# Kernel tuning notes

Hardware: AMD Instinct MI355X
Metric: run time of the kernel (lower is better)

The kernel has to match this reference:

```python
import jax, jax.numpy as jnp
import numpy as np

B, N, DIM = 4, 1024, 1024
HEADS, DH = 16, 64
INNER = HEADS * DH          # 1024
PROJ_H = max(16, DH // 8)   # 16
TOP_K = 256
TEMP = 1.0
SCALE = DH ** -0.5
LN_EPS = 1e-5


def setup_inputs() -> dict:
    key = jax.random.key(0)
    ks = jax.random.split(key, 9)
    s = 0.02
    return {
        "x": jax.random.normal(ks[0], (B, N, DIM), dtype=jnp.float32),
        "w_qkv": jax.random.normal(ks[1], (3 * INNER, DIM), dtype=jnp.float32) * s,
        "w_out": jax.random.normal(ks[2], (DIM, INNER), dtype=jnp.float32) * s,
        "b_out": jnp.zeros((DIM,), dtype=jnp.float32),
        "ln_g": jnp.ones((DH,), dtype=jnp.float32),
        "ln_b": jnp.zeros((DH,), dtype=jnp.float32),
        "w1": jax.random.normal(ks[3], (PROJ_H, DH), dtype=jnp.float32) * s,
        "b1": jnp.zeros((PROJ_H,), dtype=jnp.float32),
        "w2": jax.random.normal(ks[4], (1, PROJ_H), dtype=jnp.float32) * s,
        "b2": jnp.zeros((1,), dtype=jnp.float32),
    }


def _soma_gate(token_feat, ln_g, ln_b, w1, b1, w2, b2):
    # token_feat: [B, N, DH] -> gate [B, N] in (0,1)
    mu = token_feat.mean(axis=-1, keepdims=True)
    var = token_feat.var(axis=-1, keepdims=True)
    H = (token_feat - mu) * jax.lax.rsqrt(var + LN_EPS) * ln_g + ln_b
    h = jax.nn.gelu(H @ w1.T + b1, approximate=False)
    scores = (h @ w2.T + b2)[..., 0]                       # [B, N]
    scores = scores / (TEMP + 1e-12)
    # top-k soft mask: non-topk positions set to -1e9 before sigmoid
    topk_vals, topk_idx = jax.lax.top_k(scores, TOP_K)
    b_idx = jnp.arange(scores.shape[0])[:, None]
    scores = jnp.full_like(scores, -1e9).at[b_idx, topk_idx].set(topk_vals)
    return jax.nn.sigmoid(scores)


def reference(x, w_qkv, w_out, b_out, ln_g, ln_b, w1, b1, w2, b2):
    Bx, Nx, _ = x.shape
    qkv = x @ w_qkv.T                                      # [B, N, 3*INNER]
    q, k, v = jnp.split(qkv, 3, axis=-1)
    to_heads = lambda t: t.reshape(Bx, Nx, HEADS, DH).transpose(0, 2, 1, 3)
    q, k, v = to_heads(q), to_heads(k), to_heads(v)        # [B, H, N, DH]

    dots = jnp.einsum('bhid,bhjd->bhij', q, k) * SCALE     # [B, H, N, N]

    q_mean = q.mean(axis=1)                                # [B, N, DH]
    gate = _soma_gate(q_mean, ln_g, ln_b, w1, b1, w2, b2)  # [B, N]
    dots = dots * (gate[:, None, :, None] * gate[:, None, None, :])

    attn = jax.nn.softmax(dots, axis=-1)
    out = jnp.einsum('bhij,bhjd->bhid', attn, v)           # [B, H, N, DH]
    out = out.transpose(0, 2, 1, 3).reshape(Bx, Nx, INNER)
    return out @ w_out.T + b_out
```

## Files before the change

kernel.cpp:

```cpp
#include <hip/hip_runtime.h>
#include <hip/hip_bf16.h>
#include <stdint.h>

typedef __bf16 bf16;
typedef __bf16 bf16x8 __attribute__((ext_vector_type(8)));
typedef float floatx4 __attribute__((ext_vector_type(4)));

typedef const __attribute__((address_space(1))) uint32_t glb_u32;
typedef __attribute__((address_space(3))) uint32_t lds_u32;

__device__ __forceinline__ void cp16(void* lds, const void* gp) {
    __builtin_amdgcn_global_load_lds((glb_u32*)gp, (lds_u32*)lds, 16, 0, 0);
}

#define MFMA16(a, b, c) __builtin_amdgcn_mfma_f32_16x16x32_bf16((a), (b), (c), 0, 0, 0)
#define SCALE_ 0.125f

__global__ __launch_bounds__(256) void k_cvt_prep(
    const float* __restrict__ x, const float* __restrict__ wq,
    const float* __restrict__ wo, bf16* __restrict__ xb,
    bf16* __restrict__ wqb, bf16* __restrict__ wob,
    float* __restrict__ wqmT) {
    if (blockIdx.x < 4096) {
        size_t i8 = ((size_t)blockIdx.x * 256 + threadIdx.x) * 8;
        const float* src; bf16* dst; size_t off;
        if (i8 < 4194304)      { src = x;  dst = xb;  off = i8; }
        else if (i8 < 7340032) { src = wq; dst = wqb; off = i8 - 4194304; }
        else                   { src = wo; dst = wob; off = i8 - 7340032; }
        float4 a = *(const float4*)(src + off);
        float4 b = *(const float4*)(src + off + 4);
        union { bf16 h[8]; uint4 u; } tmp;
        tmp.h[0] = (bf16)a.x; tmp.h[1] = (bf16)a.y; tmp.h[2] = (bf16)a.z; tmp.h[3] = (bf16)a.w;
        tmp.h[4] = (bf16)b.x; tmp.h[5] = (bf16)b.y; tmp.h[6] = (bf16)b.z; tmp.h[7] = (bf16)b.w;
        *(uint4*)(dst + off) = tmp.u;
    } else {
        int t = (blockIdx.x - 4096) * 256 + threadIdx.x;
        int k = t & 1023, d = t >> 10;
        float s = 0.f;
        #pragma unroll
        for (int h = 0; h < 16; ++h) s += wq[(size_t)(h * 64 + d) * 1024 + k];
        wqmT[k * 64 + d] = s * (1.f / 16.f);
    }
}

__global__ __launch_bounds__(256) void k_score(
    const float* __restrict__ xf, const float* __restrict__ wqmT,
    const float* __restrict__ lng, const float* __restrict__ lnb,
    const float* __restrict__ w1f, const float* __restrict__ b1f,
    const float* __restrict__ w2f, const float* __restrict__ b2f,
    float* __restrict__ scores) {
    const int w = threadIdx.x >> 6, lane = threadIdx.x & 63;
    const int r0 = blockIdx.x * 8;
    const int k0 = w * 256;
    __shared__ float part[4][8][64];
    __shared__ float qm_s[8][64];
    __shared__ float Hs[4][64];
    __shared__ float hh[4][16];

    float acc[8];
    #pragma unroll
    for (int i = 0; i < 8; ++i) acc[i] = 0.f;

    for (int k = k0; k < k0 + 256; k += 4) {
        float w0 = wqmT[(k + 0) * 64 + lane];
        float w1 = wqmT[(k + 1) * 64 + lane];
        float w2 = wqmT[(k + 2) * 64 + lane];
        float w3 = wqmT[(k + 3) * 64 + lane];
        #pragma unroll
        for (int i = 0; i < 8; ++i) {
            float4 xv = *(const float4*)(xf + (size_t)(r0 + i) * 1024 + k);
            acc[i] += xv.x * w0; acc[i] += xv.y * w1;
            acc[i] += xv.z * w2; acc[i] += xv.w * w3;
        }
    }
    #pragma unroll
    for (int i = 0; i < 8; ++i) part[w][i][lane] = acc[i];
    __syncthreads();
    for (int e = threadIdx.x; e < 512; e += 256) {
        int r = e >> 6, d = e & 63;
        qm_s[r][d] = part[0][r][d] + part[1][r][d] + part[2][r][d] + part[3][r][d];
    }
    __syncthreads();

    for (int i = 0; i < 2; ++i) {
        const int r = w * 2 + i;
        float qm = qm_s[r][lane];
        float s = qm;
        #pragma unroll
        for (int off = 32; off > 0; off >>= 1) s += __shfl_xor(s, off);
        float mu = s * (1.f / 64.f);
        float dx = qm - mu;
        float v2 = dx * dx;
        #pragma unroll
        for (int off = 32; off > 0; off >>= 1) v2 += __shfl_xor(v2, off);
        float var = v2 * (1.f / 64.f);
        float H = dx * (1.0f / sqrtf(var + 1e-5f)) * lng[lane] + lnb[lane];
        Hs[w][lane] = H;
        if (lane < 16) {
            float a = b1f[lane];
            #pragma unroll
            for (int d = 0; d < 64; ++d) a += Hs[w][d] * w1f[lane * 64 + d];
            hh[w][lane] = 0.5f * a * (1.0f + erff(a * 0.70710678118654752f));
        }
        if (lane == 0) {
            float sc = b2f[0];
            #pragma unroll
            for (int p = 0; p < 16; ++p) sc += hh[w][p] * w2f[p];
            scores[r0 + r] = sc;
        }
    }
}

__global__ __launch_bounds__(256) void k_topk(const float* __restrict__ scores,
                                              float* __restrict__ gate,
                                              int* __restrict__ idx,
                                              float* __restrict__ gsel) {
    const int w = threadIdx.x >> 6, lane = threadIdx.x & 63;
    const float* sc = scores + w * 1024;
    float s[16];
    uint32_t key[16];
    #pragma unroll
    for (int i = 0; i < 16; ++i) {
        s[i] = sc[lane * 16 + i];
        uint32_t u = __float_as_uint(s[i]);
        key[i] = (u >> 31) ? ~u : (u | 0x80000000u);
    }
    uint32_t prefix = 0;
    for (int bit = 31; bit >= 0; --bit) {
        uint32_t cand = prefix | (1u << bit);
        int c = 0;
        #pragma unroll
        for (int i = 0; i < 16; ++i) c += (key[i] >= cand);
        #pragma unroll
        for (int off = 1; off < 64; off <<= 1) c += __shfl_xor(c, off);
        if (c >= 256) prefix = cand;
    }
    int cg = 0, eq = 0;
    #pragma unroll
    for (int i = 0; i < 16; ++i) { cg += (key[i] > prefix); eq += (key[i] == prefix); }
    #pragma unroll
    for (int off = 1; off < 64; off <<= 1) cg += __shfl_xor(cg, off);
    const int quota = 256 - cg;
    int xs = eq;
    #pragma unroll
    for (int off = 1; off < 64; off <<= 1) {
        int y = __shfl_up(xs, off);
        if (lane >= off) xs += y;
    }
    int run = xs - eq;
    bool selv[16];
    int cnt = 0;
    #pragma unroll
    for (int i = 0; i < 16; ++i) {
        bool sel = key[i] > prefix;
        if (key[i] == prefix) { sel = (run < quota); run++; }
        selv[i] = sel;
        cnt += sel ? 1 : 0;
        gate[w * 1024 + lane * 16 + i] = sel ? 1.0f / (1.0f + expf(-s[i])) : 0.0f;
    }
    int xc = cnt;
    #pragma unroll
    for (int off = 1; off < 64; off <<= 1) {
        int y = __shfl_up(xc, off);
        if (lane >= off) xc += y;
    }
    int pos = xc - cnt;
    #pragma unroll
    for (int i = 0; i < 16; ++i) {
        if (selv[i]) {
            idx[w * 256 + pos]  = lane * 16 + i;
            gsel[w * 256 + pos] = 1.0f / (1.0f + expf(-s[i]));
            pos++;
        }
    }
}

__global__ __launch_bounds__(256) void k_qkv_fast(
    const bf16* __restrict__ xb, const bf16* __restrict__ wqb,
    bf16* __restrict__ qbuf, bf16* __restrict__ kbuf, bf16* __restrict__ vbuf) {
    __shared__ bf16 As[128 * 32];
    __shared__ bf16 Bs[128 * 32];
    const int t = threadIdx.x;
    const int lane = t & 63;
    const int w = t >> 6;
    const int n0 = blockIdx.x * 128;
    const int m0 = blockIdx.y * 128;
    const bf16* Asrc = xb + (size_t)m0 * 1024;
    const bf16* Bsrc = wqb + (size_t)n0 * 1024;

    const int srow = t >> 2;
    const int scol = (t & 3) * 8;
    const int wm = (w & 1) * 64;
    const int wn = (w >> 1) * 64;
    const int fr = lane & 15;
    const int kc = (lane >> 4) * 8;

    floatx4 zero4 = {0.f, 0.f, 0.f, 0.f};
    floatx4 acc[4][4];
    #pragma unroll
    for (int i = 0; i < 4; ++i)
        #pragma unroll
        for (int j = 0; j < 4; ++j) acc[i][j] = zero4;

    for (int k0 = 0; k0 < 1024; k0 += 32) {
        __syncthreads();
        cp16(As + t * 8,        Asrc + (size_t)srow * 1024 + k0 + scol);
        cp16(As + t * 8 + 2048, Asrc + (size_t)(srow + 64) * 1024 + k0 + scol);
        cp16(Bs + t * 8,        Bsrc + (size_t)srow * 1024 + k0 + scol);
        cp16(Bs + t * 8 + 2048, Bsrc + (size_t)(srow + 64) * 1024 + k0 + scol);
        __syncthreads();
        bf16x8 a[4], b[4];
        #pragma unroll
        for (int mi = 0; mi < 4; ++mi)
            a[mi] = *(const bf16x8*)&As[(wm + mi * 16 + fr) * 32 + kc];
        #pragma unroll
        for (int ni = 0; ni < 4; ++ni)
            b[ni] = *(const bf16x8*)&Bs[(wn + ni * 16 + fr) * 32 + kc];
        #pragma unroll
        for (int mi = 0; mi < 4; ++mi)
            #pragma unroll
            for (int ni = 0; ni < 4; ++ni)
                acc[mi][ni] = MFMA16(a[mi], b[ni], acc[mi][ni]);
    }

    const int rowb = (lane >> 4) * 4;
    #pragma unroll
    for (int ni = 0; ni < 4; ++ni) {
        const int n_base = n0 + wn + ni * 16;
        const int region = n_base >> 10;
        const int nn = n_base & 1023;
        const int h = nn >> 6;
        const int d = (nn & 63) + fr;
        bf16* dst = (region == 0) ? qbuf : (region == 1) ? kbuf : vbuf;
        #pragma unroll
        for (int mi = 0; mi < 4; ++mi) {
            #pragma unroll
            for (int r = 0; r < 4; ++r) {
                const int mg = m0 + wm + mi * 16 + rowb + r;
                const int bb = mg >> 10;
                const int nq = mg & 1023;
                const size_t bh = (size_t)(bb * 16 + h);
                dst[(bh * 1024 + nq) * 64 + d] = (bf16)acc[mi][ni][r];
            }
        }
    }
}

__global__ __launch_bounds__(256) void k_compact(
    const bf16* __restrict__ kbuf, const bf16* __restrict__ vbuf,
    const int* __restrict__ idx, bf16* __restrict__ Ksel,
    bf16* __restrict__ VselT, float* __restrict__ SumVuns) {
    const int bh = blockIdx.x, b = bh >> 4;
    const int t = threadIdx.x, w = t >> 6, lane = t & 63;
    const bf16* kb = kbuf + (size_t)bh * 65536;
    const bf16* vb = vbuf + (size_t)bh * 65536;
    bf16* Ko = Ksel + (size_t)bh * 16384;
    bf16* Vo = VselT + (size_t)bh * 16384;

    __shared__ bf16 Vt[64][72];
    __shared__ float redAll[4][64];
    __shared__ float redSel[4][64];

    float sAll = 0.f;
    for (int j = w * 256; j < w * 256 + 256; ++j)
        sAll += (float)vb[(size_t)j * 64 + lane];
    redAll[w][lane] = sAll;

    const int d = t & 63, sg = t >> 6;
    const int s_loc = t >> 2, part = t & 3;
    float sSel = 0.f;

    for (int c = 0; c < 4; ++c) {
        __syncthreads();
        int j = idx[b * 256 + c * 64 + s_loc];
        const uint4* ksrc = (const uint4*)(kb + (size_t)j * 64 + part * 16);
        uint4* kdst = (uint4*)(Ko + (size_t)(c * 64 + s_loc) * 64 + part * 16);
        kdst[0] = ksrc[0]; kdst[1] = ksrc[1];
        const uint4* vsrc = (const uint4*)(vb + (size_t)j * 64 + part * 16);
        uint4 v0 = vsrc[0], v1 = vsrc[1];
        *(uint4*)&Vt[s_loc][part * 16]     = v0;
        *(uint4*)&Vt[s_loc][part * 16 + 8] = v1;
        __syncthreads();
        union { bf16 h[16]; uint4 u[2]; } tmp;
        #pragma unroll
        for (int u = 0; u < 16; ++u) {
            bf16 v = Vt[sg * 16 + u][d];
            tmp.h[u] = v;
            sSel += (float)v;
        }
        uint4* vdst = (uint4*)(Vo + (size_t)d * 256 + c * 64 + sg * 16);
        vdst[0] = tmp.u[0]; vdst[1] = tmp.u[1];
    }
    redSel[sg][d] = sSel;
    __syncthreads();
    if (t < 64) {
        float su = redAll[0][t] + redAll[1][t] + redAll[2][t] + redAll[3][t]
                 - (redSel[0][t] + redSel[1][t] + redSel[2][t] + redSel[3][t]);
        SumVuns[bh * 64 + t] = su;
    }
}

__global__ __launch_bounds__(256) void k_attn(
    bf16* __restrict__ qbuf, const bf16* __restrict__ Ksel,
    const bf16* __restrict__ VselT, const float* __restrict__ gate,
    const float* __restrict__ gsel, const float* __restrict__ SumVuns) {
    const int bh = blockIdx.x;
    const int qt = blockIdx.y;
    const int b = bh >> 4;
    const int t = threadIdx.x, w = t >> 6, lane = t & 63;
    const int m0 = qt * 64;
    bf16* qb = qbuf + (size_t)bh * 65536;
    const bf16* kb = Ksel + (size_t)bh * 16384;
    const bf16* vb = VselT + (size_t)bh * 16384;

    __shared__ bf16 Qs[64 * 72];
    __shared__ bf16 Ks[64 * 72];
    __shared__ bf16 Vs[64 * 72];
    __shared__ bf16 Ps[4][16 * 72];

    #pragma unroll
    for (int c = 0; c < 2; ++c) {
        int idx2 = t + 256 * c, row = idx2 >> 3, c8 = (idx2 & 7) * 8;
        *(uint4*)&Qs[row * 72 + c8] = *(const uint4*)&qb[(size_t)(m0 + row) * 64 + c8];
    }
    const int fr = lane & 15;
    const int kq = lane >> 4;
    const int rowb = kq * 4;
    __syncthreads();
    bf16x8 aq[2];
    aq[0] = *(const bf16x8*)&Qs[(w * 16 + fr) * 72 + kq * 8];
    aq[1] = *(const bf16x8*)&Qs[(w * 16 + fr) * 72 + 32 + kq * 8];

    float gq[4];
    #pragma unroll
    for (int r = 0; r < 4; ++r)
        gq[r] = gate[b * 1024 + m0 + w * 16 + rowb + r] * SCALE_;

    float mrow[4] = {0.f, 0.f, 0.f, 0.f};
    float lrow[4] = {0.f, 0.f, 0.f, 0.f};
    floatx4 zero4 = {0.f, 0.f, 0.f, 0.f};
    floatx4 Of[4] = {zero4, zero4, zero4, zero4};

    for (int jt = 0; jt < 4; ++jt) {
        const int j0 = jt * 64;
        __syncthreads();
        #pragma unroll
        for (int c = 0; c < 2; ++c) {
            int idx2 = t + 256 * c, row = idx2 >> 3, c8 = (idx2 & 7) * 8;
            *(uint4*)&Ks[row * 72 + c8] = *(const uint4*)&kb[(size_t)(j0 + row) * 64 + c8];
            *(uint4*)&Vs[row * 72 + c8] = *(const uint4*)&vb[(size_t)row * 256 + j0 + c8];
        }
        __syncthreads();

        floatx4 S[4] = {zero4, zero4, zero4, zero4};
        #pragma unroll
        for (int ks = 0; ks < 2; ++ks) {
            #pragma unroll
            for (int ni = 0; ni < 4; ++ni) {
                bf16x8 bfr = *(const bf16x8*)&Ks[(ni * 16 + fr) * 72 + ks * 32 + kq * 8];
                S[ni] = MFMA16(aq[ks], bfr, S[ni]);
            }
        }
        float gk[4];
        #pragma unroll
        for (int ni = 0; ni < 4; ++ni) gk[ni] = gsel[b * 256 + j0 + ni * 16 + fr];

        float p[4][4], rmax[4] = {0.f, 0.f, 0.f, 0.f};
        #pragma unroll
        for (int ni = 0; ni < 4; ++ni)
            #pragma unroll
            for (int r = 0; r < 4; ++r) {
                float sv = S[ni][r] * (gq[r] * gk[ni]);
                p[ni][r] = sv;
                rmax[r] = fmaxf(rmax[r], sv);
            }
        #pragma unroll
        for (int r = 0; r < 4; ++r) {
            #pragma unroll
            for (int off = 1; off < 16; off <<= 1)
                rmax[r] = fmaxf(rmax[r], __shfl_xor(rmax[r], off));
        }
        float alpha[4], rsum[4] = {0.f, 0.f, 0.f, 0.f};
        #pragma unroll
        for (int r = 0; r < 4; ++r) {
            float mn = fmaxf(mrow[r], rmax[r]);
            alpha[r] = __expf(mrow[r] - mn);
            mrow[r] = mn;
        }
        #pragma unroll
        for (int ni = 0; ni < 4; ++ni)
            #pragma unroll
            for (int r = 0; r < 4; ++r) {
                float pv = __expf(p[ni][r] - mrow[r]);
                p[ni][r] = pv;
                rsum[r] += pv;
            }
        #pragma unroll
        for (int r = 0; r < 4; ++r) {
            #pragma unroll
            for (int off = 1; off < 16; off <<= 1) rsum[r] += __shfl_xor(rsum[r], off);
            lrow[r] = lrow[r] * alpha[r] + rsum[r];
        }
        #pragma unroll
        for (int nd = 0; nd < 4; ++nd)
            #pragma unroll
            for (int r = 0; r < 4; ++r) Of[nd][r] *= alpha[r];

        #pragma unroll
        for (int ni = 0; ni < 4; ++ni)
            #pragma unroll
            for (int r = 0; r < 4; ++r)
                Ps[w][(rowb + r) * 72 + ni * 16 + fr] = (bf16)p[ni][r];

        #pragma unroll
        for (int ks = 0; ks < 2; ++ks) {
            bf16x8 ap = *(const bf16x8*)&Ps[w][fr * 72 + ks * 32 + kq * 8];
            #pragma unroll
            for (int nd = 0; nd < 4; ++nd) {
                bf16x8 bv = *(const bf16x8*)&Vs[(nd * 16 + fr) * 72 + ks * 32 + kq * 8];
                Of[nd] = MFMA16(ap, bv, Of[nd]);
            }
        }
    }

    #pragma unroll
    for (int nd = 0; nd < 4; ++nd)
        #pragma unroll
        for (int r = 0; r < 4; ++r) {
            float em = __expf(-mrow[r]);
            float num = Of[nd][r] + em * SumVuns[bh * 64 + nd * 16 + fr];
            float den = lrow[r] + 768.0f * em;
            qb[(size_t)(m0 + w * 16 + rowb + r) * 64 + nd * 16 + fr] = (bf16)(num / den);
        }
}

__global__ __launch_bounds__(256) void k_out_fast(
    const bf16* __restrict__ A, const bf16* __restrict__ wob,
    const float* __restrict__ b_out, float* __restrict__ out) {
    __shared__ bf16 As[128 * 32];
    __shared__ bf16 Bs[128 * 32];
    const int t = threadIdx.x;
    const int lane = t & 63;
    const int w = t >> 6;
    const int n0 = blockIdx.x * 128;
    const int m0 = blockIdx.y * 128;
    const bf16* Bsrc = wob + (size_t)n0 * 1024;

    const int srow = t >> 2;
    const int scol = (t & 3) * 8;
    const int wm = (w & 1) * 64;
    const int wn = (w >> 1) * 64;
    const int fr = lane & 15;
    const int kc = (lane >> 4) * 8;

    const int mg1 = m0 + srow, mg2 = m0 + srow + 64;
    const size_t abase1 = ((size_t)(mg1 >> 10) * 16 * 1024 + (mg1 & 1023)) * 64;
    const size_t abase2 = ((size_t)(mg2 >> 10) * 16 * 1024 + (mg2 & 1023)) * 64;

    floatx4 zero4 = {0.f, 0.f, 0.f, 0.f};
    floatx4 acc[4][4];
    #pragma unroll
    for (int i = 0; i < 4; ++i)
        #pragma unroll
        for (int j = 0; j < 4; ++j) acc[i][j] = zero4;

    for (int k0 = 0; k0 < 1024; k0 += 32) {
        __syncthreads();
        {
            const int kk = k0 + scol;
            const size_t hoff = (size_t)(kk >> 6) * 65536 + (kk & 63);
            cp16(As + t * 8,        A + abase1 + hoff);
            cp16(As + t * 8 + 2048, A + abase2 + hoff);
        }
        cp16(Bs + t * 8,        Bsrc + (size_t)srow * 1024 + k0 + scol);
        cp16(Bs + t * 8 + 2048, Bsrc + (size_t)(srow + 64) * 1024 + k0 + scol);
        __syncthreads();
        bf16x8 a[4], b[4];
        #pragma unroll
        for (int mi = 0; mi < 4; ++mi)
            a[mi] = *(const bf16x8*)&As[(wm + mi * 16 + fr) * 32 + kc];
        #pragma unroll
        for (int ni = 0; ni < 4; ++ni)
            b[ni] = *(const bf16x8*)&Bs[(wn + ni * 16 + fr) * 32 + kc];
        #pragma unroll
        for (int mi = 0; mi < 4; ++mi)
            #pragma unroll
            for (int ni = 0; ni < 4; ++ni)
                acc[mi][ni] = MFMA16(a[mi], b[ni], acc[mi][ni]);
    }

    const int rowb = (lane >> 4) * 4;
    #pragma unroll
    for (int ni = 0; ni < 4; ++ni) {
        const int ng = n0 + wn + ni * 16 + fr;
        const float bias = b_out[ng];
        #pragma unroll
        for (int mi = 0; mi < 4; ++mi)
            #pragma unroll
            for (int r = 0; r < 4; ++r) {
                const int mg = m0 + wm + mi * 16 + rowb + r;
                out[(size_t)mg * 1024 + ng] = acc[mi][ni][r] + bias;
            }
    }
}

extern "C" void kernel_launch(void* const* d_in, const int* in_sizes, int n_in,
                              void* d_out, int out_size, void* d_ws, size_t ws_size,
                              hipStream_t stream) {
    const float* x     = (const float*)d_in[0];
    const float* w_qkv = (const float*)d_in[1];
    const float* w_out = (const float*)d_in[2];
    const float* b_out = (const float*)d_in[3];
    const float* ln_g  = (const float*)d_in[4];
    const float* ln_b  = (const float*)d_in[5];
    const float* w1    = (const float*)d_in[6];
    const float* b1    = (const float*)d_in[7];
    const float* w2    = (const float*)d_in[8];
    const float* b2    = (const float*)d_in[9];
    float* out = (float*)d_out;

    char* ws = (char*)d_ws;
    bf16*  qbuf  = (bf16*)(ws);
    bf16*  kbuf  = (bf16*)(ws + 8388608);
    bf16*  vbuf  = (bf16*)(ws + 16777216);
    bf16*  xb    = (bf16*)(ws + 25165824);
    bf16*  wqb   = (bf16*)(ws + 33554432);
    bf16*  wob   = (bf16*)(ws + 39845888);
    bf16*  Ksel    = (bf16*)(ws + 33554432);
    bf16*  VselT   = (bf16*)(ws + 35651584);
    float* SumVuns = (float*)(ws + 37748736);
    const size_t tail = 41943040;
    float* wqmT   = (float*)(ws + tail);
    int*   idx    = (int*)(ws + tail);
    float* gsel   = (float*)(ws + tail + 4096);
    float* scores = (float*)(ws + tail + 262144);
    float* gate   = (float*)(ws + tail + 262144 + 16384);

    k_cvt_prep<<<4352, 256, 0, stream>>>(x, w_qkv, w_out, xb, wqb, wob, wqmT);
    k_score<<<512, 256, 0, stream>>>(x, wqmT, ln_g, ln_b, w1, b1, w2, b2, scores);
    k_topk<<<1, 256, 0, stream>>>(scores, gate, idx, gsel);
    k_qkv_fast<<<dim3(24, 32), 256, 0, stream>>>(xb, wqb, qbuf, kbuf, vbuf);
    k_compact<<<64, 256, 0, stream>>>(kbuf, vbuf, idx, Ksel, VselT, SumVuns);
    k_attn<<<dim3(64, 16), 256, 0, stream>>>(qbuf, Ksel, VselT, gate, gsel, SumVuns);
    k_out_fast<<<dim3(8, 32), 256, 0, stream>>>(qbuf, wob, b_out, out);
}
```

Measured before the change: 241.9 us.

## Compute Q/K projections, attention and output projection only for top-k tokens

```diff
diff --git a/kernel.cpp b/kernel.cpp
--- a/kernel.cpp
+++ b/kernel.cpp
@@ -175,19 +175,15 @@
     }
 }
 
-__global__ __launch_bounds__(256) void k_qkv_fast(
+__global__ __launch_bounds__(256) void k_qkv_sel(
     const bf16* __restrict__ xb, const bf16* __restrict__ wqb,
-    bf16* __restrict__ qbuf, bf16* __restrict__ kbuf, bf16* __restrict__ vbuf) {
+    const int* __restrict__ idx, bf16* __restrict__ qsel,
+    bf16* __restrict__ ksel, bf16* __restrict__ vbuf) {
     __shared__ bf16 As[128 * 32];
     __shared__ bf16 Bs[128 * 32];
     const int t = threadIdx.x;
     const int lane = t & 63;
     const int w = t >> 6;
-    const int n0 = blockIdx.x * 128;
-    const int m0 = blockIdx.y * 128;
-    const bf16* Asrc = xb + (size_t)m0 * 1024;
-    const bf16* Bsrc = wqb + (size_t)n0 * 1024;
-
     const int srow = t >> 2;
     const int scol = (t & 3) * 8;
     const int wm = (w & 1) * 64;
@@ -195,6 +191,29 @@
     const int fr = lane & 15;
     const int kc = (lane >> 4) * 8;
 
+    const int bid = blockIdx.x;
+    const bool isV = bid < 256;
+    int n0, m0;
+    size_t abase1, abase2;
+    const bf16* Bsrc;
+    if (isV) {
+        n0 = (bid & 7) * 128;
+        m0 = (bid >> 3) * 128;
+        Bsrc = wqb + (size_t)(2048 + n0) * 1024;
+        abase1 = (size_t)(m0 + srow) * 1024;
+        abase2 = (size_t)(m0 + srow + 64) * 1024;
+    } else {
+        int q = bid - 256;
+        n0 = (q & 15) * 128;
+        m0 = (q >> 4) * 128;
+        Bsrc = wqb + (size_t)n0 * 1024;
+        const int mg1 = m0 + srow, mg2 = mg1 + 64;
+        const int tok1 = idx[(mg1 >> 8) * 256 + (mg1 & 255)];
+        const int tok2 = idx[(mg2 >> 8) * 256 + (mg2 & 255)];
+        abase1 = ((size_t)(mg1 >> 8) * 1024 + tok1) * 1024;
+        abase2 = ((size_t)(mg2 >> 8) * 1024 + tok2) * 1024;
+    }
+
     floatx4 zero4 = {0.f, 0.f, 0.f, 0.f};
     floatx4 acc[4][4];
     #pragma unroll
@@ -204,8 +223,8 @@
 
     for (int k0 = 0; k0 < 1024; k0 += 32) {
         __syncthreads();
-        cp16(As + t * 8,        Asrc + (size_t)srow * 1024 + k0 + scol);
-        cp16(As + t * 8 + 2048, Asrc + (size_t)(srow + 64) * 1024 + k0 + scol);
+        cp16(As + t * 8,        xb + abase1 + k0 + scol);
+        cp16(As + t * 8 + 2048, xb + abase2 + k0 + scol);
         cp16(Bs + t * 8,        Bsrc + (size_t)srow * 1024 + k0 + scol);
         cp16(Bs + t * 8 + 2048, Bsrc + (size_t)(srow + 64) * 1024 + k0 + scol);
         __syncthreads();
@@ -227,34 +246,47 @@
     #pragma unroll
     for (int ni = 0; ni < 4; ++ni) {
         const int n_base = n0 + wn + ni * 16;
-        const int region = n_base >> 10;
-        const int nn = n_base & 1023;
-        const int h = nn >> 6;
-        const int d = (nn & 63) + fr;
-        bf16* dst = (region == 0) ? qbuf : (region == 1) ? kbuf : vbuf;
-        #pragma unroll
-        for (int mi = 0; mi < 4; ++mi) {
-            #pragma unroll
-            for (int r = 0; r < 4; ++r) {
-                const int mg = m0 + wm + mi * 16 + rowb + r;
-                const int bb = mg >> 10;
-                const int nq = mg & 1023;
-                const size_t bh = (size_t)(bb * 16 + h);
-                dst[(bh * 1024 + nq) * 64 + d] = (bf16)acc[mi][ni][r];
-            }
-        }
-    }
-}
-
-__global__ __launch_bounds__(256) void k_compact(
-    const bf16* __restrict__ kbuf, const bf16* __restrict__ vbuf,
-    const int* __restrict__ idx, bf16* __restrict__ Ksel,
-    bf16* __restrict__ VselT, float* __restrict__ SumVuns) {
-    const int bh = blockIdx.x, b = bh >> 4;
+        if (isV) {
+            const int h = n_base >> 6;
+            const int dd = (n_base & 63) + fr;
+            #pragma unroll
+            for (int mi = 0; mi < 4; ++mi)
+                #pragma unroll
+                for (int r = 0; r < 4; ++r) {
+                    const int mg = m0 + wm + mi * 16 + rowb + r;
+                    const int bb = mg >> 10, nq = mg & 1023;
+                    vbuf[(((size_t)(bb * 16 + h)) * 1024 + nq) * 64 + dd] =
+                        (bf16)acc[mi][ni][r];
+                }
+        } else {
+            const int region = n_base >> 10;
+            const int nn = n_base & 1023;
+            const int h = nn >> 6;
+            const int dd = (nn & 63) + fr;
+            #pragma unroll
+            for (int mi = 0; mi < 4; ++mi)
+                #pragma unroll
+                for (int r = 0; r < 4; ++r) {
+                    const int mg = m0 + wm + mi * 16 + rowb + r;
+                    const bf16 v = (bf16)acc[mi][ni][r];
+                    if (region == 0) {
+                        qsel[(size_t)mg * 1024 + h * 64 + dd] = v;
+                    } else {
+                        const int b = mg >> 8, s = mg & 255;
+                        ksel[(((size_t)(b * 16 + h)) * 256 + s) * 64 + dd] = v;
+                    }
+                }
+        }
+    }
+}
+
+__global__ __launch_bounds__(256) void k_vgather(
+    const bf16* __restrict__ vbuf, const int* __restrict__ idx,
+    bf16* __restrict__ VselT, float* __restrict__ SumVuns,
+    bf16* __restrict__ qsel) {
+    const int bh = blockIdx.x, b = bh >> 4, h = bh & 15;
     const int t = threadIdx.x, w = t >> 6, lane = t & 63;
-    const bf16* kb = kbuf + (size_t)bh * 65536;
     const bf16* vb = vbuf + (size_t)bh * 65536;
-    bf16* Ko = Ksel + (size_t)bh * 16384;
     bf16* Vo = VselT + (size_t)bh * 16384;
 
     __shared__ bf16 Vt[64][72];
@@ -273,19 +305,16 @@
     for (int c = 0; c < 4; ++c) {
         __syncthreads();
         int j = idx[b * 256 + c * 64 + s_loc];
-        const uint4* ksrc = (const uint4*)(kb + (size_t)j * 64 + part * 16);
-        uint4* kdst = (uint4*)(Ko + (size_t)(c * 64 + s_loc) * 64 + part * 16);
-        kdst[0] = ksrc[0]; kdst[1] = ksrc[1];
         const uint4* vsrc = (const uint4*)(vb + (size_t)j * 64 + part * 16);
         uint4 v0 = vsrc[0], v1 = vsrc[1];
         *(uint4*)&Vt[s_loc][part * 16]     = v0;
         *(uint4*)&Vt[s_loc][part * 16 + 8] = v1;
         __syncthreads();
-        union { bf16 h[16]; uint4 u[2]; } tmp;
+        union { bf16 h_[16]; uint4 u[2]; } tmp;
         #pragma unroll
         for (int u = 0; u < 16; ++u) {
             bf16 v = Vt[sg * 16 + u][d];
-            tmp.h[u] = v;
+            tmp.h_[u] = v;
             sSel += (float)v;
         }
         uint4* vdst = (uint4*)(Vo + (size_t)d * 256 + c * 64 + sg * 16);
@@ -294,22 +323,22 @@
     redSel[sg][d] = sSel;
     __syncthreads();
     if (t < 64) {
-        float su = redAll[0][t] + redAll[1][t] + redAll[2][t] + redAll[3][t]
-                 - (redSel[0][t] + redSel[1][t] + redSel[2][t] + redSel[3][t]);
-        SumVuns[bh * 64 + t] = su;
+        float sa = redAll[0][t] + redAll[1][t] + redAll[2][t] + redAll[3][t];
+        float ss = redSel[0][t] + redSel[1][t] + redSel[2][t] + redSel[3][t];
+        SumVuns[bh * 64 + t] = sa - ss;
+        qsel[(size_t)(1024 + b) * 1024 + h * 64 + t] = (bf16)(sa * (1.f / 1024.f));
     }
 }
 
 __global__ __launch_bounds__(256) void k_attn(
-    bf16* __restrict__ qbuf, const bf16* __restrict__ Ksel,
-    const bf16* __restrict__ VselT, const float* __restrict__ gate,
-    const float* __restrict__ gsel, const float* __restrict__ SumVuns) {
+    bf16* __restrict__ qsel, const bf16* __restrict__ Ksel,
+    const bf16* __restrict__ VselT, const float* __restrict__ gsel,
+    const float* __restrict__ SumVuns) {
     const int bh = blockIdx.x;
     const int qt = blockIdx.y;
-    const int b = bh >> 4;
+    const int b = bh >> 4, h = bh & 15;
     const int t = threadIdx.x, w = t >> 6, lane = t & 63;
     const int m0 = qt * 64;
-    bf16* qb = qbuf + (size_t)bh * 65536;
     const bf16* kb = Ksel + (size_t)bh * 16384;
     const bf16* vb = VselT + (size_t)bh * 16384;
 
@@ -321,7 +350,8 @@
     #pragma unroll
     for (int c = 0; c < 2; ++c) {
         int idx2 = t + 256 * c, row = idx2 >> 3, c8 = (idx2 & 7) * 8;
-        *(uint4*)&Qs[row * 72 + c8] = *(const uint4*)&qb[(size_t)(m0 + row) * 64 + c8];
+        *(uint4*)&Qs[row * 72 + c8] =
+            *(const uint4*)&qsel[(size_t)(b * 256 + m0 + row) * 1024 + h * 64 + c8];
     }
     const int fr = lane & 15;
     const int kq = lane >> 4;
@@ -334,7 +364,7 @@
     float gq[4];
     #pragma unroll
     for (int r = 0; r < 4; ++r)
-        gq[r] = gate[b * 1024 + m0 + w * 16 + rowb + r] * SCALE_;
+        gq[r] = gsel[b * 256 + m0 + w * 16 + rowb + r] * SCALE_;
 
     float mrow[4] = {0.f, 0.f, 0.f, 0.f};
     float lrow[4] = {0.f, 0.f, 0.f, 0.f};
@@ -430,13 +460,15 @@
             float em = __expf(-mrow[r]);
             float num = Of[nd][r] + em * SumVuns[bh * 64 + nd * 16 + fr];
             float den = lrow[r] + 768.0f * em;
-            qb[(size_t)(m0 + w * 16 + rowb + r) * 64 + nd * 16 + fr] = (bf16)(num / den);
-        }
-}
-
-__global__ __launch_bounds__(256) void k_out_fast(
+            qsel[(size_t)(b * 256 + m0 + w * 16 + rowb + r) * 1024 +
+                 h * 64 + nd * 16 + fr] = (bf16)(num / den);
+        }
+}
+
+__global__ __launch_bounds__(256) void k_out_sel(
     const bf16* __restrict__ A, const bf16* __restrict__ wob,
-    const float* __restrict__ b_out, float* __restrict__ out) {
+    const float* __restrict__ b_out, const int* __restrict__ idx,
+    float* __restrict__ ubase, float* __restrict__ out) {
     __shared__ bf16 As[128 * 32];
     __shared__ bf16 Bs[128 * 32];
     const int t = threadIdx.x;
@@ -453,10 +485,6 @@
     const int fr = lane & 15;
     const int kc = (lane >> 4) * 8;
 
-    const int mg1 = m0 + srow, mg2 = m0 + srow + 64;
-    const size_t abase1 = ((size_t)(mg1 >> 10) * 16 * 1024 + (mg1 & 1023)) * 64;
-    const size_t abase2 = ((size_t)(mg2 >> 10) * 16 * 1024 + (mg2 & 1023)) * 64;
-
     floatx4 zero4 = {0.f, 0.f, 0.f, 0.f};
     floatx4 acc[4][4];
     #pragma unroll
@@ -466,12 +494,8 @@
 
     for (int k0 = 0; k0 < 1024; k0 += 32) {
         __syncthreads();
-        {
-            const int kk = k0 + scol;
-            const size_t hoff = (size_t)(kk >> 6) * 65536 + (kk & 63);
-            cp16(As + t * 8,        A + abase1 + hoff);
-            cp16(As + t * 8 + 2048, A + abase2 + hoff);
-        }
+        cp16(As + t * 8,        A + (size_t)(m0 + srow) * 1024 + k0 + scol);
+        cp16(As + t * 8 + 2048, A + (size_t)(m0 + srow + 64) * 1024 + k0 + scol);
         cp16(Bs + t * 8,        Bsrc + (size_t)srow * 1024 + k0 + scol);
         cp16(Bs + t * 8 + 2048, Bsrc + (size_t)(srow + 64) * 1024 + k0 + scol);
         __syncthreads();
@@ -499,9 +523,26 @@
             #pragma unroll
             for (int r = 0; r < 4; ++r) {
                 const int mg = m0 + wm + mi * 16 + rowb + r;
-                out[(size_t)mg * 1024 + ng] = acc[mi][ni][r] + bias;
+                const float val = acc[mi][ni][r] + bias;
+                if (mg < 1024) {
+                    const int b = mg >> 8, s = mg & 255;
+                    const int tok = idx[b * 256 + s];
+                    out[((size_t)b * 1024 + tok) * 1024 + ng] = val;
+                } else if (mg < 1028) {
+                    ubase[(size_t)(mg - 1024) * 1024 + ng] = val;
+                }
             }
     }
+}
+
+__global__ __launch_bounds__(256) void k_fill(
+    const float* __restrict__ gate, const float* __restrict__ ubase,
+    float* __restrict__ out) {
+    const int tokg = blockIdx.x;
+    if (gate[tokg] > 0.f) return;
+    const int b = tokg >> 10;
+    const int c = threadIdx.x * 4;
+    *(float4*)(out + (size_t)tokg * 1024 + c) = *(const float4*)(ubase + b * 1024 + c);
 }
 
 extern "C" void kernel_launch(void* const* d_in, const int* in_sizes, int n_in,
@@ -520,27 +561,27 @@
     float* out = (float*)d_out;
 
     char* ws = (char*)d_ws;
-    bf16*  qbuf  = (bf16*)(ws);
-    bf16*  kbuf  = (bf16*)(ws + 8388608);
-    bf16*  vbuf  = (bf16*)(ws + 16777216);
-    bf16*  xb    = (bf16*)(ws + 25165824);
-    bf16*  wqb   = (bf16*)(ws + 33554432);
-    bf16*  wob   = (bf16*)(ws + 39845888);
-    bf16*  Ksel    = (bf16*)(ws + 33554432);
-    bf16*  VselT   = (bf16*)(ws + 35651584);
-    float* SumVuns = (float*)(ws + 37748736);
-    const size_t tail = 41943040;
-    float* wqmT   = (float*)(ws + tail);
-    int*   idx    = (int*)(ws + tail);
-    float* gsel   = (float*)(ws + tail + 4096);
-    float* scores = (float*)(ws + tail + 262144);
-    float* gate   = (float*)(ws + tail + 262144 + 16384);
+    bf16*  qsel  = (bf16*)(ws);
+    bf16*  ksel  = (bf16*)(ws + 4194304);
+    bf16*  VselT = (bf16*)(ws + 6291456);
+    bf16*  vbuf  = (bf16*)(ws + 8388608);
+    bf16*  xb    = (bf16*)(ws + 16777216);
+    bf16*  wqb   = (bf16*)(ws + 25165824);
+    bf16*  wob   = (bf16*)(ws + 31457280);
+    float* wqmT    = (float*)(ws + 33554432);
+    int*   idx     = (int*)(ws + 33816576);
+    float* gsel    = (float*)(ws + 33820672);
+    float* scores  = (float*)(ws + 33824768);
+    float* gate    = (float*)(ws + 33841152);
+    float* SumVuns = (float*)(ws + 33857536);
+    float* ubase   = (float*)(ws + 33873920);
 
     k_cvt_prep<<<4352, 256, 0, stream>>>(x, w_qkv, w_out, xb, wqb, wob, wqmT);
     k_score<<<512, 256, 0, stream>>>(x, wqmT, ln_g, ln_b, w1, b1, w2, b2, scores);
     k_topk<<<1, 256, 0, stream>>>(scores, gate, idx, gsel);
-    k_qkv_fast<<<dim3(24, 32), 256, 0, stream>>>(xb, wqb, qbuf, kbuf, vbuf);
-    k_compact<<<64, 256, 0, stream>>>(kbuf, vbuf, idx, Ksel, VselT, SumVuns);
-    k_attn<<<dim3(64, 16), 256, 0, stream>>>(qbuf, Ksel, VselT, gate, gsel, SumVuns);
-    k_out_fast<<<dim3(8, 32), 256, 0, stream>>>(qbuf, wob, b_out, out);
-}
+    k_qkv_sel<<<384, 256, 0, stream>>>(xb, wqb, idx, qsel, ksel, vbuf);
+    k_vgather<<<64, 256, 0, stream>>>(vbuf, idx, VselT, SumVuns, qsel);
+    k_attn<<<dim3(64, 4), 256, 0, stream>>>(qsel, ksel, VselT, gsel, SumVuns);
+    k_out_sel<<<dim3(8, 9), 256, 0, stream>>>(qsel, wob, b_out, idx, ubase, out);
+    k_fill<<<4096, 256, 0, stream>>>(gate, ubase, out);
+}
```

Result: no change. 237.2 us (-2.0%).
